# Optimization experiments

Hardware: AMD Instinct MI355X
Metric: run time of the kernel (lower is better)

Reference implementation:

```python
import jax, jax.numpy as jnp
import numpy as np
from itertools import permutations, product

K = 64
RADIUS = 0.15


def generate_24_rotations():
    # All signed permutation matrices with det=+1: the 24 rotations of the cube.
    mats = []
    for perm in permutations(range(3)):
        for signs in product([1.0, -1.0], repeat=3):
            M = np.zeros((3, 3), dtype=np.float32)
            for r in range(3):
                M[r, perm[r]] = signs[r]
            if np.linalg.det(M) > 0:
                mats.append(M)
    return jnp.asarray(np.stack(mats))  # [24, 3, 3]


def ball_group(x, y, k, radius):
    # x: [B, N, 3] queries, y: [B, M, 3] support points.
    # Returns relative coords of k neighbors within radius: [B, N, k, 3].
    d2 = jnp.sum((x[:, :, None, :] - y[:, None, :, :]) ** 2, axis=-1)  # [B,N,M]
    masked = jnp.where(d2 <= radius * radius, -d2, -jnp.inf)
    vals, idx = jax.lax.top_k(masked, k)                 # k nearest within ball
    nearest = jnp.argmin(d2, axis=-1)                    # fallback: global nearest
    idx = jnp.where(vals > -jnp.inf, idx, nearest[:, :, None])  # [B,N,k]
    gathered = jnp.take_along_axis(y[:, None, :, :],
                                   idx[:, :, :, None], axis=2)  # [B,N,k,3]
    return gathered - x[:, :, None, :]


def setup_inputs() -> dict:
    key = jax.random.key(0)
    kx, k1, k2, k3, k4 = jax.random.split(key, 5)
    B, N = 2, 1024
    x = jax.random.uniform(kx, (B, N, 3), dtype=jnp.float32)  # unit cube
    W1 = jax.random.normal(k1, (32, 3), dtype=jnp.float32) * 0.1
    b1 = jax.random.normal(k2, (32,), dtype=jnp.float32) * 0.1
    W2 = jax.random.normal(k3, (64, 32), dtype=jnp.float32) * 0.1
    b2 = jax.random.normal(k4, (64,), dtype=jnp.float32) * 0.1
    return {"x": x, "W1": W1, "b1": b1, "W2": W2, "b2": b2}


def reference(x, W1, b1, W2, b2):
    Rs = generate_24_rotations()  # [24,3,3]
    gp = ball_group(x, x, K, RADIUS)  # [B,N,K,3]
    # Faithful to torch.einsum('bnkj,ijj->bnikj', ...): repeated j takes the
    # DIAGONAL of each rotation matrix: out = gp[...,j] * Rs[i,j,j].
    gp = jnp.einsum('bnkj,ijj->bnikj', gp, Rs)       # [B,N,24,K,3]
    gp = jnp.transpose(gp, (0, 4, 1, 2, 3))          # [B,3,N,24,K]
    # 1x1x1 Conv3d == pointwise linear over channel dim, then ReLU.
    h = jax.nn.relu(jnp.einsum('bcnik,oc->bonik', gp, W1)
                    + b1[None, :, None, None, None])  # [B,32,N,24,K]
    h = jax.nn.relu(jnp.einsum('bcnik,oc->bonik', h, W2)
                    + b2[None, :, None, None, None])  # [B,64,N,24,K]
    f = jnp.max(h, axis=-1)   # max over neighbors  -> [B,64,N,24]
    f = jnp.mean(f, axis=-1)  # mean over rotations -> [B,64,N]
    return f
```

## Files before the change

kernel.cpp:

```cpp
#include <hip/hip_runtime.h>
#include <math.h>

typedef _Float16 half8 __attribute__((ext_vector_type(8)));
typedef float    f32x4 __attribute__((ext_vector_type(4)));

#define NPTS 1024
#define KMAX 64
#define R2   0.0225f

__global__ __launch_bounds__(256, 4) void point_encoder_kernel(
    const float* __restrict__ xg,
    const float* __restrict__ W1g,
    const float* __restrict__ b1g,
    const float* __restrict__ W2g,
    const float* __restrict__ b2g,
    float* __restrict__ outg)
{
    __shared__ float nb[KMAX * 3];
    __shared__ int   cnt;

    const int tid  = threadIdx.x;
    const int nt   = tid >> 6;
    const int lane = tid & 63;
    const int kl   = lane & 15;
    const int quad = lane >> 4;

    const int b = blockIdx.x >> 10;
    const int n = blockIdx.x & (NPTS - 1);

    const int o = nt * 16 + kl;
    const f32x4 w2a = *(const f32x4*)(W2g + o * 32 + quad * 8);
    const f32x4 w2b = *(const f32x4*)(W2g + o * 32 + quad * 8 + 4);
    const float b2v = b2g[o];
    f32x4 w1raw[6];
    #pragma unroll
    for (int j = 0; j < 6; ++j)
        w1raw[j] = *(const f32x4*)(W1g + quad * 24 + j * 4);
    const f32x4 b1a = *(const f32x4*)(b1g + quad * 8);
    const f32x4 b1b = *(const f32x4*)(b1g + quad * 8 + 4);

    if (tid < KMAX * 3) nb[tid] = 0.f;
    if (tid == 0)       cnt = 0;
    __syncthreads();

    const float* xb = xg + b * NPTS * 3;
    const float qx = xb[n*3+0], qy = xb[n*3+1], qz = xb[n*3+2];
    #pragma unroll
    for (int it = 0; it < 4; ++it) {
        const int idx = nt * 256 + it * 64 + lane;
        const float dx = xb[idx*3+0] - qx;
        const float dy = xb[idx*3+1] - qy;
        const float dz = xb[idx*3+2] - qz;
        const float d2 = dx*dx + dy*dy + dz*dz;
        const bool pred = (d2 <= R2);
        const unsigned long long mask = __ballot(pred);
        const int cit = __popcll(mask);
        int base0 = 0;
        if (lane == 0 && cit) base0 = atomicAdd(&cnt, cit);
        base0 = __shfl(base0, 0, 64);
        const int pos = base0 + __popcll(mask & ((1ull << lane) - 1ull));
        if (pred && pos < KMAX) {
            nb[pos*3+0] = dx; nb[pos*3+1] = dy; nb[pos*3+2] = dz;
        }
    }
    __syncthreads();
    int cn = cnt; if (cn > KMAX) cn = KMAX;
    const int ntiles = (cn + 15) >> 4;

    half8 Bf;
    #pragma unroll
    for (int j = 0; j < 4; ++j) {
        Bf[j]     = (_Float16)w2a[j];
        Bf[j + 4] = (_Float16)w2b[j];
    }
    float w1x[8], w1y[8], w1z[8], b1r[8];
    #pragma unroll
    for (int j = 0; j < 8; ++j) {
        w1x[j] = w1raw[(j*3    ) >> 2][(j*3    ) & 3];
        w1y[j] = w1raw[(j*3 + 1) >> 2][(j*3 + 1) & 3];
        w1z[j] = w1raw[(j*3 + 2) >> 2][(j*3 + 2) & 3];
        b1r[j] = (j < 4) ? b1a[j] : b1b[j - 4];
    }

    half8 Ac;
    #pragma unroll
    for (int j = 0; j < 8; ++j) Ac[j] = (_Float16)fmaxf(b1r[j], 0.f);
    f32x4 Cc = {0.f, 0.f, 0.f, 0.f};
    Cc = __builtin_amdgcn_mfma_f32_16x16x32_f16(Ac, Bf, Cc, 0, 0, 0);
    float acc = 8.f * fmaxf(Cc[0] + b2v, 0.f);

    float mv[10];
    #pragma unroll
    for (int i = 0; i < 10; ++i) mv[i] = -INFINITY;

    for (int mt = 0; mt < ntiles; ++mt) {
        const int k = mt * 16 + kl;
        const float gx = nb[k*3+0], gy = nb[k*3+1], gz = nb[k*3+2];
        half8 A[10];
        #pragma unroll
        for (int j = 0; j < 8; ++j) {
            const float tx = w1x[j] * gx;
            const float ty = w1y[j] * gy;
            const float tz = w1z[j] * gz;
            const float pxy = tx + ty, mxy = tx - ty;
            const float bpz = b1r[j] + tz, bmz = b1r[j] - tz;
            A[0][j] = (_Float16)fmaxf(bpz + pxy, 0.f);
            A[1][j] = (_Float16)fmaxf(bmz + mxy, 0.f);
            A[2][j] = (_Float16)fmaxf(bmz - mxy, 0.f);
            A[3][j] = (_Float16)fmaxf(bpz - pxy, 0.f);
            A[4][j] = (_Float16)fmaxf(b1r[j] + tx, 0.f);
            A[5][j] = (_Float16)fmaxf(b1r[j] - tx, 0.f);
            A[6][j] = (_Float16)fmaxf(b1r[j] + ty, 0.f);
            A[7][j] = (_Float16)fmaxf(b1r[j] - ty, 0.f);
            A[8][j] = (_Float16)fmaxf(bpz, 0.f);
            A[9][j] = (_Float16)fmaxf(bmz, 0.f);
        }
        #pragma unroll
        for (int i = 0; i < 10; ++i) {
            f32x4 C = {0.f, 0.f, 0.f, 0.f};
            C = __builtin_amdgcn_mfma_f32_16x16x32_f16(A[i], Bf, C, 0, 0, 0);
            mv[i] = fmaxf(mv[i], fmaxf(fmaxf(C[0], C[1]), fmaxf(C[2], C[3])));
        }
    }

    #pragma unroll
    for (int i = 0; i < 10; ++i) {
        float r = mv[i];
        r = fmaxf(r, __shfl_xor(r, 16, 64));
        r = fmaxf(r, __shfl_xor(r, 32, 64));
        acc += ((i < 4) ? 1.f : 2.f) * fmaxf(r + b2v, 0.f);
    }
    if (quad == 0)
        outg[(size_t)b * (64 * NPTS) + (size_t)o * NPTS + n] = acc * (1.f / 24.f);
}

extern "C" void kernel_launch(void* const* d_in, const int* in_sizes, int n_in,
                              void* d_out, int out_size, void* d_ws, size_t ws_size,
                              hipStream_t stream) {
    const float* x  = (const float*)d_in[0];
    const float* W1 = (const float*)d_in[1];
    const float* b1 = (const float*)d_in[2];
    const float* W2 = (const float*)d_in[3];
    const float* b2 = (const float*)d_in[4];
    float* out = (float*)d_out;

    const int total = in_sizes[0] / 3;
    point_encoder_kernel<<<total, 256, 0, stream>>>(x, W1, b1, W2, b2, out);
}
```

Before: 74.47 us.

## Process multiple query points per block to amortize weight setup

Each block now uses 1024 threads in four independent 256-thread groups, and each group handles two query points in turn, so one block covers eight points. The per-thread weight loads, fp16 conversion and the constant bias MFMA are done once per block rather than once per point. Groups share block-wide barriers, so a group with many neighbours can stall the others. The larger blocks also cut the launch from 2048 blocks to 256, which may leave compute units under-filled.

```diff
diff --git a/kernel.cpp b/kernel.cpp
--- a/kernel.cpp
+++ b/kernel.cpp
@@ -7,8 +7,10 @@
 #define NPTS 1024
 #define KMAX 64
 #define R2   0.0225f
+#define GRPS 4
+#define REPS 2
 
-__global__ __launch_bounds__(256, 4) void point_encoder_kernel(
+__global__ __launch_bounds__(1024, 4) void point_encoder_kernel(
     const float* __restrict__ xg,
     const float* __restrict__ W1g,
     const float* __restrict__ b1g,
@@ -16,17 +18,16 @@
     const float* __restrict__ b2g,
     float* __restrict__ outg)
 {
-    __shared__ float nb[KMAX * 3];
-    __shared__ int   cnt;
+    __shared__ float nb[GRPS][KMAX * 3];
+    __shared__ int   scnt[GRPS];
 
     const int tid  = threadIdx.x;
-    const int nt   = tid >> 6;
+    const int grp  = tid >> 8;
+    const int t    = tid & 255;
+    const int nt   = t >> 6;
     const int lane = tid & 63;
     const int kl   = lane & 15;
     const int quad = lane >> 4;
-
-    const int b = blockIdx.x >> 10;
-    const int n = blockIdx.x & (NPTS - 1);
 
     const int o = nt * 16 + kl;
     const f32x4 w2a = *(const f32x4*)(W2g + o * 32 + quad * 8);
@@ -38,34 +39,6 @@
         w1raw[j] = *(const f32x4*)(W1g + quad * 24 + j * 4);
     const f32x4 b1a = *(const f32x4*)(b1g + quad * 8);
     const f32x4 b1b = *(const f32x4*)(b1g + quad * 8 + 4);
-
-    if (tid < KMAX * 3) nb[tid] = 0.f;
-    if (tid == 0)       cnt = 0;
-    __syncthreads();
-
-    const float* xb = xg + b * NPTS * 3;
-    const float qx = xb[n*3+0], qy = xb[n*3+1], qz = xb[n*3+2];
-    #pragma unroll
-    for (int it = 0; it < 4; ++it) {
-        const int idx = nt * 256 + it * 64 + lane;
-        const float dx = xb[idx*3+0] - qx;
-        const float dy = xb[idx*3+1] - qy;
-        const float dz = xb[idx*3+2] - qz;
-        const float d2 = dx*dx + dy*dy + dz*dz;
-        const bool pred = (d2 <= R2);
-        const unsigned long long mask = __ballot(pred);
-        const int cit = __popcll(mask);
-        int base0 = 0;
-        if (lane == 0 && cit) base0 = atomicAdd(&cnt, cit);
-        base0 = __shfl(base0, 0, 64);
-        const int pos = base0 + __popcll(mask & ((1ull << lane) - 1ull));
-        if (pred && pos < KMAX) {
-            nb[pos*3+0] = dx; nb[pos*3+1] = dy; nb[pos*3+2] = dz;
-        }
-    }
-    __syncthreads();
-    int cn = cnt; if (cn > KMAX) cn = KMAX;
-    const int ntiles = (cn + 15) >> 4;
 
     half8 Bf;
     #pragma unroll
@@ -87,51 +60,91 @@
     for (int j = 0; j < 8; ++j) Ac[j] = (_Float16)fmaxf(b1r[j], 0.f);
     f32x4 Cc = {0.f, 0.f, 0.f, 0.f};
     Cc = __builtin_amdgcn_mfma_f32_16x16x32_f16(Ac, Bf, Cc, 0, 0, 0);
-    float acc = 8.f * fmaxf(Cc[0] + b2v, 0.f);
+    const float cbase = 8.f * fmaxf(Cc[0] + b2v, 0.f);
 
-    float mv[10];
-    #pragma unroll
-    for (int i = 0; i < 10; ++i) mv[i] = -INFINITY;
+    for (int rep = 0; rep < REPS; ++rep) {
+        const int pt = blockIdx.x * (GRPS * REPS) + rep * GRPS + grp;
+        const int b  = pt >> 10;
+        const int n  = pt & (NPTS - 1);
 
-    for (int mt = 0; mt < ntiles; ++mt) {
-        const int k = mt * 16 + kl;
-        const float gx = nb[k*3+0], gy = nb[k*3+1], gz = nb[k*3+2];
-        half8 A[10];
+        __syncthreads();
+        if (t < KMAX * 3) nb[grp][t] = 0.f;
+        if (t == 0)       scnt[grp] = 0;
+        __syncthreads();
+
+        const float* xb = xg + b * NPTS * 3;
+        const float qx = xb[n*3+0], qy = xb[n*3+1], qz = xb[n*3+2];
         #pragma unroll
-        for (int j = 0; j < 8; ++j) {
-            const float tx = w1x[j] * gx;
-            const float ty = w1y[j] * gy;
-            const float tz = w1z[j] * gz;
-            const float pxy = tx + ty, mxy = tx - ty;
-            const float bpz = b1r[j] + tz, bmz = b1r[j] - tz;
-            A[0][j] = (_Float16)fmaxf(bpz + pxy, 0.f);
-            A[1][j] = (_Float16)fmaxf(bmz + mxy, 0.f);
-            A[2][j] = (_Float16)fmaxf(bmz - mxy, 0.f);
-            A[3][j] = (_Float16)fmaxf(bpz - pxy, 0.f);
-            A[4][j] = (_Float16)fmaxf(b1r[j] + tx, 0.f);
-            A[5][j] = (_Float16)fmaxf(b1r[j] - tx, 0.f);
-            A[6][j] = (_Float16)fmaxf(b1r[j] + ty, 0.f);
-            A[7][j] = (_Float16)fmaxf(b1r[j] - ty, 0.f);
-            A[8][j] = (_Float16)fmaxf(bpz, 0.f);
-            A[9][j] = (_Float16)fmaxf(bmz, 0.f);
+        for (int it = 0; it < 4; ++it) {
+            const int idx = nt * 256 + it * 64 + lane;
+            const float dx = xb[idx*3+0] - qx;
+            const float dy = xb[idx*3+1] - qy;
+            const float dz = xb[idx*3+2] - qz;
+            const float d2 = dx*dx + dy*dy + dz*dz;
+            const bool pred = (d2 <= R2);
+            const unsigned long long mask = __ballot(pred);
+            const int cit = __popcll(mask);
+            int base0 = 0;
+            if (lane == 0 && cit) base0 = atomicAdd(&scnt[grp], cit);
+            base0 = __shfl(base0, 0, 64);
+            const int pos = base0 + __popcll(mask & ((1ull << lane) - 1ull));
+            if (pred && pos < KMAX) {
+                nb[grp][pos*3+0] = dx;
+                nb[grp][pos*3+1] = dy;
+                nb[grp][pos*3+2] = dz;
+            }
         }
+        __syncthreads();
+        int cn = scnt[grp]; if (cn > KMAX) cn = KMAX;
+        const int ntiles = (cn + 15) >> 4;
+
+        float acc = cbase;
+        float mv[10];
+        #pragma unroll
+        for (int i = 0; i < 10; ++i) mv[i] = -INFINITY;
+
+        for (int mt = 0; mt < ntiles; ++mt) {
+            const int k = mt * 16 + kl;
+            const float gx = nb[grp][k*3+0];
+            const float gy = nb[grp][k*3+1];
+            const float gz = nb[grp][k*3+2];
+            half8 A[10];
+            #pragma unroll
+            for (int j = 0; j < 8; ++j) {
+                const float tx = w1x[j] * gx;
+                const float ty = w1y[j] * gy;
+                const float tz = w1z[j] * gz;
+                const float pxy = tx + ty, mxy = tx - ty;
+                const float bpz = b1r[j] + tz, bmz = b1r[j] - tz;
+                A[0][j] = (_Float16)fmaxf(bpz + pxy, 0.f);
+                A[1][j] = (_Float16)fmaxf(bmz + mxy, 0.f);
+                A[2][j] = (_Float16)fmaxf(bmz - mxy, 0.f);
+                A[3][j] = (_Float16)fmaxf(bpz - pxy, 0.f);
+                A[4][j] = (_Float16)fmaxf(b1r[j] + tx, 0.f);
+                A[5][j] = (_Float16)fmaxf(b1r[j] - tx, 0.f);
+                A[6][j] = (_Float16)fmaxf(b1r[j] + ty, 0.f);
+                A[7][j] = (_Float16)fmaxf(b1r[j] - ty, 0.f);
+                A[8][j] = (_Float16)fmaxf(bpz, 0.f);
+                A[9][j] = (_Float16)fmaxf(bmz, 0.f);
+            }
+            #pragma unroll
+            for (int i = 0; i < 10; ++i) {
+                f32x4 C = {0.f, 0.f, 0.f, 0.f};
+                C = __builtin_amdgcn_mfma_f32_16x16x32_f16(A[i], Bf, C, 0, 0, 0);
+                mv[i] = fmaxf(mv[i], fmaxf(fmaxf(C[0], C[1]), fmaxf(C[2], C[3])));
+            }
+        }
+
         #pragma unroll
         for (int i = 0; i < 10; ++i) {
-            f32x4 C = {0.f, 0.f, 0.f, 0.f};
-            C = __builtin_amdgcn_mfma_f32_16x16x32_f16(A[i], Bf, C, 0, 0, 0);
-            mv[i] = fmaxf(mv[i], fmaxf(fmaxf(C[0], C[1]), fmaxf(C[2], C[3])));
+            float r = mv[i];
+            r = fmaxf(r, __shfl_xor(r, 16, 64));
+            r = fmaxf(r, __shfl_xor(r, 32, 64));
+            acc += ((i < 4) ? 1.f : 2.f) * fmaxf(r + b2v, 0.f);
         }
+        if (quad == 0)
+            outg[(size_t)b * (64 * NPTS) + (size_t)o * NPTS + n] = acc * (1.f / 24.f);
     }
-
-    #pragma unroll
-    for (int i = 0; i < 10; ++i) {
-        float r = mv[i];
-        r = fmaxf(r, __shfl_xor(r, 16, 64));
-        r = fmaxf(r, __shfl_xor(r, 32, 64));
-        acc += ((i < 4) ? 1.f : 2.f) * fmaxf(r + b2v, 0.f);
-    }
-    if (quad == 0)
-        outg[(size_t)b * (64 * NPTS) + (size_t)o * NPTS + n] = acc * (1.f / 24.f);
 }
 
 extern "C" void kernel_launch(void* const* d_in, const int* in_sizes, int n_in,
@@ -144,6 +157,7 @@
     const float* b2 = (const float*)d_in[4];
     float* out = (float*)d_out;
 
-    const int total = in_sizes[0] / 3;
-    point_encoder_kernel<<<total, 256, 0, stream>>>(x, W1, b1, W2, b2, out);
+    const int total  = in_sizes[0] / 3;
+    const int blocks = total / (GRPS * REPS);
+    point_encoder_kernel<<<blocks, 1024, 0, stream>>>(x, W1, b1, W2, b2, out);
 }
```

After: 82.44 us. +10.7%, slower.
